# Kernel tuning notes

Hardware: AMD Instinct MI355X
Metric: run time of the kernel (lower is better)

The kernel has to match this reference:

```python
import jax, jax.numpy as jnp
import numpy as np

N_NODES = 100000
N_EDGES = 600000
N_GRAPHS = 64
BN_EPS = 1e-5


def setup_inputs() -> dict:
    key = jax.random.key(0)
    ks = jax.random.split(key, 32)
    inp = {
        "x": jax.random.normal(ks[0], (N_NODES, 128), dtype=jnp.float32),
        "edge_index": jax.random.randint(ks[1], (2, N_EDGES), 0, N_NODES, dtype=jnp.int64),
        "batch": jnp.sort(jax.random.randint(ks[2], (N_NODES,), 0, N_GRAPHS, dtype=jnp.int64)),
    }
    dims = [(128, 64, 64), (64, 64, 64), (64, 64, 96)]  # (in, hid, out) per GIN layer
    ki = 3
    for i, (d_in, d_hid, d_out) in enumerate(dims):
        inp[f"l{i}_w1"] = jax.random.normal(ks[ki], (d_in, d_hid), dtype=jnp.float32) * 0.05; ki += 1
        inp[f"l{i}_b1"] = jnp.zeros((d_hid,), dtype=jnp.float32)
        inp[f"l{i}_w2"] = jax.random.normal(ks[ki], (d_hid, d_out), dtype=jnp.float32) * 0.05; ki += 1
        inp[f"l{i}_b2"] = jnp.zeros((d_out,), dtype=jnp.float32)
        inp[f"bn{i}_g"] = jax.random.uniform(ks[ki], (d_out,), minval=0.5, maxval=1.5, dtype=jnp.float32); ki += 1
        inp[f"bn{i}_b"] = jax.random.normal(ks[ki], (d_out,), dtype=jnp.float32) * 0.05; ki += 1
        inp[f"bn{i}_m"] = jax.random.normal(ks[ki], (d_out,), dtype=jnp.float32) * 0.05; ki += 1
        inp[f"bn{i}_v"] = jax.random.uniform(ks[ki], (d_out,), minval=0.5, maxval=1.5, dtype=jnp.float32); ki += 1
    return inp


def _gin_layer(x, src, dst, w1, b1, w2, b2, g, bb, m, v):
    # GINConv (eps=0): h_i = MLP(x_i + sum_{j: j->i} x_j)
    aggr = jax.ops.segment_sum(x[src], dst, num_segments=N_NODES)
    h = x + aggr
    h = jax.nn.relu(h @ w1 + b1) @ w2 + b2
    # eval-mode BatchNorm1d + ReLU
    h = (h - m) * jax.lax.rsqrt(v + BN_EPS) * g + bb
    return jax.nn.relu(h)


def reference(x, edge_index, batch,
              l0_w1, l0_b1, l0_w2, l0_b2, bn0_g, bn0_b, bn0_m, bn0_v,
              l1_w1, l1_b1, l1_w2, l1_b2, bn1_g, bn1_b, bn1_m, bn1_v,
              l2_w1, l2_b1, l2_w2, l2_b2, bn2_g, bn2_b, bn2_m, bn2_v):
    src, dst = edge_index[0], edge_index[1]
    h = _gin_layer(x, src, dst, l0_w1, l0_b1, l0_w2, l0_b2, bn0_g, bn0_b, bn0_m, bn0_v)
    h = _gin_layer(h, src, dst, l1_w1, l1_b1, l1_w2, l1_b2, bn1_g, bn1_b, bn1_m, bn1_v)
    h = _gin_layer(h, src, dst, l2_w1, l2_b1, l2_w2, l2_b2, bn2_g, bn2_b, bn2_m, bn2_v)
    # global mean pool over graphs
    sums = jax.ops.segment_sum(h, batch, num_segments=N_GRAPHS)
    counts = jax.ops.segment_sum(jnp.ones((h.shape[0],), dtype=h.dtype), batch, num_segments=N_GRAPHS)
    return sums / jnp.maximum(counts, 1.0)[:, None]
```

## Files before the change

kernel.cpp:

```cpp
#include <hip/hip_runtime.h>

#define N_NODES 100000
#define N_GRAPHS 64
#define N_EDGES 600000
#define BN_EPS 1e-5f

__global__ void deg_hist_kernel(const int* __restrict__ dst,
                                int* __restrict__ deg, int n_edges) {
    int e = blockIdx.x * blockDim.x + threadIdx.x;
    if (e < n_edges) atomicAdd(&deg[dst[e]], 1);
}

__global__ void scan1_kernel(const int* __restrict__ deg, int* __restrict__ excl,
                             int* __restrict__ partials, int n) {
    __shared__ int s[1024];
    int i = blockIdx.x * 1024 + threadIdx.x;
    int v = (i < n) ? deg[i] : 0;
    s[threadIdx.x] = v;
    __syncthreads();
    for (int off = 1; off < 1024; off <<= 1) {
        int t = (threadIdx.x >= (unsigned)off) ? s[threadIdx.x - off] : 0;
        __syncthreads();
        s[threadIdx.x] += t;
        __syncthreads();
    }
    if (i < n) excl[i] = s[threadIdx.x] - v;
    if (threadIdx.x == 1023) partials[blockIdx.x] = s[1023];
}

__global__ void scan2_kernel(int* partials, int nb) {
    __shared__ int s[128];
    int t = threadIdx.x;
    int v = (t < nb) ? partials[t] : 0;
    s[t] = v;
    __syncthreads();
    for (int off = 1; off < 128; off <<= 1) {
        int u = (t >= off) ? s[t - off] : 0;
        __syncthreads();
        s[t] += u;
        __syncthreads();
    }
    if (t < nb) partials[t] = s[t] - v;
}

__global__ void scan3_kernel(int* __restrict__ rowptr, const int* __restrict__ partials,
                             int n, int total) {
    int i = blockIdx.x * blockDim.x + threadIdx.x;
    if (i < n) rowptr[i] += partials[i >> 10];
    else if (i == n) rowptr[n] = total;
}

__global__ void csr_fill_kernel(const int* __restrict__ src, const int* __restrict__ dst,
                                const int* __restrict__ rowptr, int* __restrict__ cursor,
                                int* __restrict__ eids, int n_edges) {
    int e = blockIdx.x * blockDim.x + threadIdx.x;
    if (e >= n_edges) return;
    int t = dst[e];
    int pos = rowptr[t] + atomicAdd(&cursor[t], 1);
    eids[pos] = src[e];
}

__global__ void graph_bounds_kernel(const int* __restrict__ batch,
                                    int* __restrict__ gstart, int n_nodes) {
    int n = blockIdx.x * blockDim.x + threadIdx.x;
    if (n >= n_nodes) return;
    if (n == 0) {
        for (int g = 0; g <= batch[0]; ++g) gstart[g] = 0;
    } else {
        int b0 = batch[n - 1], b1 = batch[n];
        for (int g = b0 + 1; g <= b1; ++g) gstart[g] = n;
    }
    if (n == n_nodes - 1) {
        for (int g = batch[n] + 1; g <= N_GRAPHS; ++g) gstart[g] = n_nodes;
    }
}

__global__ void prep_kernel(const float* __restrict__ w1, const float* __restrict__ w2,
                            const float* __restrict__ b2, const float* __restrict__ g,
                            const float* __restrict__ bb, const float* __restrict__ m,
                            const float* __restrict__ v,
                            float* __restrict__ w1T, float* __restrict__ w2sT,
                            float* __restrict__ bias2, int DIN, int DOUT) {
    int i = blockIdx.x * blockDim.x + threadIdx.x;
    if (i < 64 * DIN) {
        int j = i / DIN, k = i % DIN;
        w1T[i] = w1[k * 64 + j];
    }
    int i2 = i - 64 * DIN;
    if (i2 >= 0 && i2 < DOUT * 64) {
        int c = i2 / 64, j = i2 % 64;
        float s = g[c] * rsqrtf(v[c] + BN_EPS);
        w2sT[i2] = w2[j * DOUT + c] * s;
    }
    int i3 = i2 - DOUT * 64;
    if (i3 >= 0 && i3 < DOUT) {
        float s = g[i3] * rsqrtf(v[i3] + BN_EPS);
        bias2[i3] = (b2[i3] - m[i3]) * s + bb[i3];
    }
}

__global__ __launch_bounds__(256)
void pre_gemm_kernel(const float* __restrict__ x, const float* __restrict__ w1T,
                     float* __restrict__ y, int n_nodes) {
    __shared__ float w1s[64 * 128];
    const int tid = threadIdx.x;
    const long base = (long)blockIdx.x * 64;

    const float4* gw1 = (const float4*)w1T;
    for (int i4 = tid; i4 < 16 * 128; i4 += 256) {
        int row = i4 >> 5, k4 = i4 & 31;
        *(float4*)&w1s[row * 128 + ((k4 ^ ((row >> 2) & 7)) << 2)] = gw1[i4];
    }
    __syncthreads();

    const int jg = tid & 15, ng = tid >> 4, xw = jg & 7;
    const float* wp = &w1s[(jg * 4) * 128];
    const float4* xv = (const float4*)x;
    long r[4];
    #pragma unroll
    for (int i = 0; i < 4; ++i) {
        long rr = base + ng * 4 + i;
        r[i] = (rr < n_nodes) ? rr : (n_nodes - 1);
    }
    float acc[4][4] = {};
    #pragma unroll 4
    for (int k4 = 0; k4 < 32; ++k4) {
        const int ko = (k4 ^ xw) << 2;
        float4 w0 = *(const float4*)&wp[0 * 128 + ko];
        float4 w1v = *(const float4*)&wp[1 * 128 + ko];
        float4 w2v = *(const float4*)&wp[2 * 128 + ko];
        float4 w3v = *(const float4*)&wp[3 * 128 + ko];
        #pragma unroll
        for (int i = 0; i < 4; ++i) {
            float4 a = xv[r[i] * 32 + k4];
            acc[i][0] = fmaf(a.x, w0.x, fmaf(a.y, w0.y, fmaf(a.z, w0.z, fmaf(a.w, w0.w, acc[i][0]))));
            acc[i][1] = fmaf(a.x, w1v.x, fmaf(a.y, w1v.y, fmaf(a.z, w1v.z, fmaf(a.w, w1v.w, acc[i][1]))));
            acc[i][2] = fmaf(a.x, w2v.x, fmaf(a.y, w2v.y, fmaf(a.z, w2v.z, fmaf(a.w, w2v.w, acc[i][2]))));
            acc[i][3] = fmaf(a.x, w3v.x, fmaf(a.y, w3v.y, fmaf(a.z, w3v.z, fmaf(a.w, w3v.w, acc[i][3]))));
        }
    }
    #pragma unroll
    for (int i = 0; i < 4; ++i) {
        long n = base + ng * 4 + i;
        if (n < n_nodes) {
            float4 v = {acc[i][0], acc[i][1], acc[i][2], acc[i][3]};
            *(float4*)(y + n * 64 + jg * 4) = v;
        }
    }
}

__global__ __launch_bounds__(256)
void gather64_kernel(const float* __restrict__ y, const int* __restrict__ rowptr,
                     const int* __restrict__ eids, const float* __restrict__ b1,
                     float* __restrict__ t, int n_nodes) {
    int node = blockIdx.x * 16 + (threadIdx.x >> 4);
    if (node >= n_nodes) return;
    int f4 = threadIdx.x & 15;
    const float4* yv = (const float4*)y;
    float4 acc = yv[(long)node * 16 + f4];
    int b = rowptr[node], e = rowptr[node + 1];
    int i = b;
    for (; i + 3 < e; i += 4) {
        int s0 = eids[i], s1 = eids[i + 1], s2 = eids[i + 2], s3 = eids[i + 3];
        float4 r0 = yv[(long)s0 * 16 + f4];
        float4 r1 = yv[(long)s1 * 16 + f4];
        float4 r2 = yv[(long)s2 * 16 + f4];
        float4 r3 = yv[(long)s3 * 16 + f4];
        acc.x += (r0.x + r1.x) + (r2.x + r3.x);
        acc.y += (r0.y + r1.y) + (r2.y + r3.y);
        acc.z += (r0.z + r1.z) + (r2.z + r3.z);
        acc.w += (r0.w + r1.w) + (r2.w + r3.w);
    }
    for (; i < e; ++i) {
        int s = eids[i];
        float4 r = yv[(long)s * 16 + f4];
        acc.x += r.x; acc.y += r.y; acc.z += r.z; acc.w += r.w;
    }
    float4 bv = ((const float4*)b1)[f4];
    float4 o;
    o.x = fmaxf(acc.x + bv.x, 0.0f);
    o.y = fmaxf(acc.y + bv.y, 0.0f);
    o.z = fmaxf(acc.z + bv.z, 0.0f);
    o.w = fmaxf(acc.w + bv.w, 0.0f);
    ((float4*)t)[(long)node * 16 + f4] = o;
}

__global__ __launch_bounds__(256)
void fused_mid_kernel(const float* __restrict__ t, const float* __restrict__ w2sT,
                      const float* __restrict__ bias2, const float* __restrict__ w1nT,
                      float* __restrict__ ynext, int n_nodes) {
    constexpr int SS = 68;
    __shared__ float sT[64 * SS];
    __shared__ float wbuf[64 * 64];
    const int tid = threadIdx.x;
    const long base = (long)blockIdx.x * 64;

    const float4* gw2 = (const float4*)w2sT;
    for (int i4 = tid; i4 < 16 * 64; i4 += 256) {
        int row = i4 >> 4, k4 = i4 & 15;
        *(float4*)&wbuf[row * 64 + ((k4 ^ ((row >> 2) & 7)) << 2)] = gw2[i4];
    }
    __syncthreads();

    const int jg = tid & 15, ng = tid >> 4, xw = jg & 7;
    const float4* tv = (const float4*)(t + base * 64);

    float h[4][4];
    {
        const float* wp = &wbuf[(jg * 4) * 64];
        float acc[4][4] = {};
        #pragma unroll 4
        for (int k4 = 0; k4 < 16; ++k4) {
            const int ko = (k4 ^ xw) << 2;
            float4 w0 = *(const float4*)&wp[0 * 64 + ko];
            float4 w1v = *(const float4*)&wp[1 * 64 + ko];
            float4 w2v = *(const float4*)&wp[2 * 64 + ko];
            float4 w3v = *(const float4*)&wp[3 * 64 + ko];
            #pragma unroll
            for (int i = 0; i < 4; ++i) {
                float4 a = tv[(ng * 4 + i) * 16 + k4];
                acc[i][0] = fmaf(a.x, w0.x, fmaf(a.y, w0.y, fmaf(a.z, w0.z, fmaf(a.w, w0.w, acc[i][0]))));
                acc[i][1] = fmaf(a.x, w1v.x, fmaf(a.y, w1v.y, fmaf(a.z, w1v.z, fmaf(a.w, w1v.w, acc[i][1]))));
                acc[i][2] = fmaf(a.x, w2v.x, fmaf(a.y, w2v.y, fmaf(a.z, w2v.z, fmaf(a.w, w2v.w, acc[i][2]))));
                acc[i][3] = fmaf(a.x, w3v.x, fmaf(a.y, w3v.y, fmaf(a.z, w3v.z, fmaf(a.w, w3v.w, acc[i][3]))));
            }
        }
        float4 bv = *(const float4*)&bias2[jg * 4];
        #pragma unroll
        for (int i = 0; i < 4; ++i) {
            h[i][0] = fmaxf(acc[i][0] + bv.x, 0.0f);
            h[i][1] = fmaxf(acc[i][1] + bv.y, 0.0f);
            h[i][2] = fmaxf(acc[i][2] + bv.z, 0.0f);
            h[i][3] = fmaxf(acc[i][3] + bv.w, 0.0f);
        }
    }
    __syncthreads();

    #pragma unroll
    for (int i = 0; i < 4; ++i) {
        float4 hv = {h[i][0], h[i][1], h[i][2], h[i][3]};
        *(float4*)&sT[(ng * 4 + i) * SS + jg * 4] = hv;
    }
    const float4* gw1n = (const float4*)w1nT;
    for (int i4 = tid; i4 < 16 * 64; i4 += 256) {
        int row = i4 >> 4, k4 = i4 & 15;
        *(float4*)&wbuf[row * 64 + ((k4 ^ ((row >> 2) & 7)) << 2)] = gw1n[i4];
    }
    __syncthreads();

    {
        const float* ap = &sT[(ng * 4) * SS];
        const float* wp = &wbuf[(jg * 4) * 64];
        float acc[4][4] = {};
        #pragma unroll 4
        for (int k4 = 0; k4 < 16; ++k4) {
            const int ko = (k4 ^ xw) << 2;
            float4 w0 = *(const float4*)&wp[0 * 64 + ko];
            float4 w1v = *(const float4*)&wp[1 * 64 + ko];
            float4 w2v = *(const float4*)&wp[2 * 64 + ko];
            float4 w3v = *(const float4*)&wp[3 * 64 + ko];
            #pragma unroll
            for (int i = 0; i < 4; ++i) {
                float4 a = *(const float4*)&ap[i * SS + k4 * 4];
                acc[i][0] = fmaf(a.x, w0.x, fmaf(a.y, w0.y, fmaf(a.z, w0.z, fmaf(a.w, w0.w, acc[i][0]))));
                acc[i][1] = fmaf(a.x, w1v.x, fmaf(a.y, w1v.y, fmaf(a.z, w1v.z, fmaf(a.w, w1v.w, acc[i][1]))));
                acc[i][2] = fmaf(a.x, w2v.x, fmaf(a.y, w2v.y, fmaf(a.z, w2v.z, fmaf(a.w, w2v.w, acc[i][2]))));
                acc[i][3] = fmaf(a.x, w3v.x, fmaf(a.y, w3v.y, fmaf(a.z, w3v.z, fmaf(a.w, w3v.w, acc[i][3]))));
            }
        }
        #pragma unroll
        for (int i = 0; i < 4; ++i) {
            long n = base + ng * 4 + i;
            if (n < n_nodes) {
                float4 v = {acc[i][0], acc[i][1], acc[i][2], acc[i][3]};
                *(float4*)(ynext + n * 64 + jg * 4) = v;
            }
        }
    }
}

__global__ __launch_bounds__(256)
void fused_final_kernel(const float* __restrict__ t, const float* __restrict__ w2sT,
                        const float* __restrict__ bias2, float* __restrict__ out,
                        int n_nodes) {
    constexpr int CPT = 6;
    __shared__ float w2s[96 * 64];
    const int tid = threadIdx.x;
    const long base = (long)blockIdx.x * 64;

    const float4* gw2 = (const float4*)w2sT;
    for (int i4 = tid; i4 < 96 * 16; i4 += 256) {
        int row = i4 >> 4, k4 = i4 & 15;
        *(float4*)&w2s[row * 64 + ((k4 ^ ((row / CPT) & 7)) << 2)] = gw2[i4];
    }
    __syncthreads();

    const int cg = tid & 15, ng = tid >> 4, xw = cg & 7;
    const float4* tv = (const float4*)(t + base * 64);
    const float* wp = &w2s[(cg * CPT) * 64];
    float acc[4][CPT] = {};
    #pragma unroll 4
    for (int k4 = 0; k4 < 16; ++k4) {
        const int ko = (k4 ^ xw) << 2;
        float4 wv[CPT];
        #pragma unroll
        for (int c = 0; c < CPT; ++c) wv[c] = *(const float4*)&wp[c * 64 + ko];
        #pragma unroll
        for (int i = 0; i < 4; ++i) {
            float4 h = tv[(ng * 4 + i) * 16 + k4];
            #pragma unroll
            for (int c = 0; c < CPT; ++c)
                acc[i][c] = fmaf(h.x, wv[c].x, fmaf(h.y, wv[c].y, fmaf(h.z, wv[c].z, fmaf(h.w, wv[c].w, acc[i][c]))));
        }
    }
    float bv[CPT];
    #pragma unroll
    for (int c = 0; c < CPT; ++c) bv[c] = bias2[cg * CPT + c];
    #pragma unroll
    for (int i = 0; i < 4; ++i) {
        long n = base + ng * 4 + i;
        if (n < n_nodes) {
            float* op = out + n * 96 + cg * CPT;
            #pragma unroll
            for (int c = 0; c < CPT; ++c) op[c] = fmaxf(acc[i][c] + bv[c], 0.0f);
        }
    }
}

#define POOL_SPLIT 16
__global__ __launch_bounds__(192)
void pool_seg_kernel(const float* __restrict__ h, const int* __restrict__ gstart,
                     float* __restrict__ sums) {
    int g = blockIdx.x >> 4;
    int s = blockIdx.x & 15;
    int lo = gstart[g], hi = gstart[g + 1];
    int len = hi - lo;
    int seg = (len + POOL_SPLIT - 1) / POOL_SPLIT;
    int a = lo + s * seg;
    int b = a + seg; if (b > hi) b = hi;

    int f4 = threadIdx.x % 24;
    int chain = threadIdx.x / 24;
    const float4* hv = (const float4*)h;
    float4 acc = {0.0f, 0.0f, 0.0f, 0.0f};
    for (int n = a + chain; n < b; n += 8) {
        float4 v = hv[(long)n * 24 + f4];
        acc.x += v.x; acc.y += v.y; acc.z += v.z; acc.w += v.w;
    }
    __shared__ float4 red[8][24];
    red[chain][f4] = acc;
    __syncthreads();
    if (threadIdx.x < 24) {
        float4 t = red[0][threadIdx.x];
        #pragma unroll
        for (int c = 1; c < 8; ++c) {
            float4 r = red[c][threadIdx.x];
            t.x += r.x; t.y += r.y; t.z += r.z; t.w += r.w;
        }
        float* sp = &sums[g * 96 + threadIdx.x * 4];
        atomicAdd(sp + 0, t.x);
        atomicAdd(sp + 1, t.y);
        atomicAdd(sp + 2, t.z);
        atomicAdd(sp + 3, t.w);
    }
}

__global__ void finalize_kernel(const float* __restrict__ sums,
                                const int* __restrict__ gstart,
                                float* __restrict__ out) {
    int i = blockIdx.x * blockDim.x + threadIdx.x;
    if (i >= N_GRAPHS * 96) return;
    int g = i / 96;
    float cnt = (float)(gstart[g + 1] - gstart[g]);
    out[i] = sums[i] / fmaxf(cnt, 1.0f);
}

static inline int cdiv_l(long a, int b) { return (int)((a + b - 1) / b); }

extern "C" void kernel_launch(void* const* d_in, const int* in_sizes, int n_in,
                              void* d_out, int out_size, void* d_ws, size_t ws_size,
                              hipStream_t stream) {
    const float* x     = (const float*)d_in[0];
    const int*   ei    = (const int*)d_in[1];
    const int*   src   = ei;
    const int*   dst   = ei + N_EDGES;
    const int*   batch = (const int*)d_in[2];

    const float* P[3][8];
    int p = 3;
    for (int l = 0; l < 3; ++l)
        for (int q = 0; q < 8; ++q)
            P[l][q] = (const float*)d_in[p++];

    const long NP = N_NODES + 64;
    float* ws   = (float*)d_ws;
    float* yT   = ws;
    float* gB   = yT + NP * 64;
    float* h2   = gB + NP * 64;
    float* q    = h2 + NP * 96;
    float* w1T[3], *w2sT[3], *bias2[3];
    for (int l = 0; l < 3; ++l) {
        w1T[l] = q;   q += 64 * 128;
        w2sT[l] = q;  q += 96 * 64;
        bias2[l] = q; q += 96;
    }
    float* sums   = q;
    int* gstart   = (int*)(sums + N_GRAPHS * 96);
    int* deg      = gstart + 72;
    int* cursor   = deg + N_NODES;
    int* partials = cursor + N_NODES;
    int* rowptr   = partials + 128;
    int* eids     = rowptr + (N_NODES + 1);

    const int B = 256;
    const int DIN[3]  = {128, 64, 64};
    const int DOUT[3] = {64, 64, 96};

    for (int l = 0; l < 3; ++l) {
        int tot = 64 * DIN[l] + 64 * DOUT[l] + DOUT[l];
        prep_kernel<<<cdiv_l(tot, B), B, 0, stream>>>(
            P[l][0], P[l][2], P[l][3], P[l][4], P[l][5], P[l][6], P[l][7],
            w1T[l], w2sT[l], bias2[l], DIN[l], DOUT[l]);
    }

    hipMemsetAsync(deg, 0, (size_t)(2 * N_NODES + 128) * sizeof(int), stream);
    deg_hist_kernel<<<cdiv_l(N_EDGES, B), B, 0, stream>>>(dst, deg, N_EDGES);
    int nblk = cdiv_l(N_NODES, 1024);
    scan1_kernel<<<nblk, 1024, 0, stream>>>(deg, rowptr, partials, N_NODES);
    scan2_kernel<<<1, 128, 0, stream>>>(partials, nblk);
    scan3_kernel<<<cdiv_l(N_NODES + 1, B), B, 0, stream>>>(rowptr, partials, N_NODES, N_EDGES);
    csr_fill_kernel<<<cdiv_l(N_EDGES, B), B, 0, stream>>>(src, dst, rowptr, cursor, eids, N_EDGES);
    graph_bounds_kernel<<<cdiv_l(N_NODES, B), B, 0, stream>>>(batch, gstart, N_NODES);

    const int ntiles = cdiv_l(N_NODES, 64);
    const int ngather = cdiv_l(N_NODES, 16);

    pre_gemm_kernel<<<ntiles, 256, 0, stream>>>(x, w1T[0], yT, N_NODES);
    gather64_kernel<<<ngather, 256, 0, stream>>>(yT, rowptr, eids, P[0][1], gB, N_NODES);
    fused_mid_kernel<<<ntiles, 256, 0, stream>>>(
        gB, w2sT[0], bias2[0], w1T[1], yT, N_NODES);
    gather64_kernel<<<ngather, 256, 0, stream>>>(yT, rowptr, eids, P[1][1], gB, N_NODES);
    fused_mid_kernel<<<ntiles, 256, 0, stream>>>(
        gB, w2sT[1], bias2[1], w1T[2], yT, N_NODES);
    gather64_kernel<<<ngather, 256, 0, stream>>>(yT, rowptr, eids, P[2][1], gB, N_NODES);
    fused_final_kernel<<<ntiles, 256, 0, stream>>>(
        gB, w2sT[2], bias2[2], h2, N_NODES);

    hipMemsetAsync(sums, 0, (size_t)(N_GRAPHS * 96) * sizeof(float), stream);
    pool_seg_kernel<<<N_GRAPHS * POOL_SPLIT, 192, 0, stream>>>(h2, gstart, sums);
    finalize_kernel<<<cdiv_l(N_GRAPHS * 96, B), B, 0, stream>>>(
        sums, gstart, (float*)d_out);
}
```

Before: 433.4 us.

## Store gathered features in bf16 and merge small setup kernels

The intermediate per-node features that the gather kernels read are now written and read as bf16, which halves the bytes fetched in the random-access neighbour gathers. The three per-layer prep kernels become one 2D-grid launch, and the CSR fill and graph-bounds kernels are merged into one. Pooling writes per-block partials instead of using atomics and a memset, and finalize sums those partials. The bf16 storage adds rounding error to the aggregated activations, and y is now double-buffered.

New measurement: 395.1 us. 1.1x faster.

```diff
diff --git a/kernel.cpp b/kernel.cpp
--- a/kernel.cpp
+++ b/kernel.cpp
@@ -4,6 +4,28 @@
 #define N_GRAPHS 64
 #define N_EDGES 600000
 #define BN_EPS 1e-5f
+
+typedef unsigned short bf16_t;
+
+__device__ __forceinline__ unsigned short f2bf(float f) {
+    unsigned int u = __float_as_uint(f);
+    u += 0x7FFF + ((u >> 16) & 1);
+    return (unsigned short)(u >> 16);
+}
+__device__ __forceinline__ float4 bf2f4(uint2 p) {
+    float4 r;
+    r.x = __uint_as_float(p.x << 16);
+    r.y = __uint_as_float(p.x & 0xFFFF0000u);
+    r.z = __uint_as_float(p.y << 16);
+    r.w = __uint_as_float(p.y & 0xFFFF0000u);
+    return r;
+}
+__device__ __forceinline__ uint2 pack4(float a, float b, float c, float d) {
+    uint2 p;
+    p.x = (unsigned)f2bf(a) | ((unsigned)f2bf(b) << 16);
+    p.y = (unsigned)f2bf(c) | ((unsigned)f2bf(d) << 16);
+    return p;
+}
 
 __global__ void deg_hist_kernel(const int* __restrict__ dst,
                                 int* __restrict__ deg, int n_edges) {
@@ -50,58 +72,59 @@
     else if (i == n) rowptr[n] = total;
 }
 
-__global__ void csr_fill_kernel(const int* __restrict__ src, const int* __restrict__ dst,
-                                const int* __restrict__ rowptr, int* __restrict__ cursor,
-                                int* __restrict__ eids, int n_edges) {
+__global__ void fill_bounds_kernel(const int* __restrict__ src, const int* __restrict__ dst,
+                                   const int* __restrict__ rowptr, int* __restrict__ cursor,
+                                   int* __restrict__ eids, const int* __restrict__ batch,
+                                   int* __restrict__ gstart, int n_edges, int n_nodes) {
     int e = blockIdx.x * blockDim.x + threadIdx.x;
-    if (e >= n_edges) return;
-    int t = dst[e];
-    int pos = rowptr[t] + atomicAdd(&cursor[t], 1);
-    eids[pos] = src[e];
-}
-
-__global__ void graph_bounds_kernel(const int* __restrict__ batch,
-                                    int* __restrict__ gstart, int n_nodes) {
-    int n = blockIdx.x * blockDim.x + threadIdx.x;
-    if (n >= n_nodes) return;
-    if (n == 0) {
-        for (int g = 0; g <= batch[0]; ++g) gstart[g] = 0;
-    } else {
-        int b0 = batch[n - 1], b1 = batch[n];
-        for (int g = b0 + 1; g <= b1; ++g) gstart[g] = n;
-    }
-    if (n == n_nodes - 1) {
-        for (int g = batch[n] + 1; g <= N_GRAPHS; ++g) gstart[g] = n_nodes;
-    }
-}
-
-__global__ void prep_kernel(const float* __restrict__ w1, const float* __restrict__ w2,
-                            const float* __restrict__ b2, const float* __restrict__ g,
-                            const float* __restrict__ bb, const float* __restrict__ m,
-                            const float* __restrict__ v,
-                            float* __restrict__ w1T, float* __restrict__ w2sT,
-                            float* __restrict__ bias2, int DIN, int DOUT) {
+    if (e < n_edges) {
+        int t = dst[e];
+        int pos = rowptr[t] + atomicAdd(&cursor[t], 1);
+        eids[pos] = src[e];
+    }
+    if (e < n_nodes) {
+        if (e == 0) {
+            for (int g = 0; g <= batch[0]; ++g) gstart[g] = 0;
+        } else {
+            int b0 = batch[e - 1], b1 = batch[e];
+            for (int g = b0 + 1; g <= b1; ++g) gstart[g] = e;
+        }
+        if (e == n_nodes - 1) {
+            for (int g = batch[e] + 1; g <= N_GRAPHS; ++g) gstart[g] = n_nodes;
+        }
+    }
+}
+
+struct LayerPrep {
+    const float *w1, *w2, *b2, *g, *bb, *m, *v;
+    float *w1T, *w2sT, *bias2;
+    int DIN, DOUT;
+};
+struct PrepAll { LayerPrep l[3]; };
+
+__global__ void prep_all_kernel(PrepAll pa) {
+    LayerPrep P = pa.l[blockIdx.y];
     int i = blockIdx.x * blockDim.x + threadIdx.x;
-    if (i < 64 * DIN) {
-        int j = i / DIN, k = i % DIN;
-        w1T[i] = w1[k * 64 + j];
-    }
-    int i2 = i - 64 * DIN;
-    if (i2 >= 0 && i2 < DOUT * 64) {
+    if (i < 64 * P.DIN) {
+        int j = i / P.DIN, k = i % P.DIN;
+        P.w1T[i] = P.w1[k * 64 + j];
+    }
+    int i2 = i - 64 * P.DIN;
+    if (i2 >= 0 && i2 < P.DOUT * 64) {
         int c = i2 / 64, j = i2 % 64;
-        float s = g[c] * rsqrtf(v[c] + BN_EPS);
-        w2sT[i2] = w2[j * DOUT + c] * s;
-    }
-    int i3 = i2 - DOUT * 64;
-    if (i3 >= 0 && i3 < DOUT) {
-        float s = g[i3] * rsqrtf(v[i3] + BN_EPS);
-        bias2[i3] = (b2[i3] - m[i3]) * s + bb[i3];
+        float s = P.g[c] * rsqrtf(P.v[c] + BN_EPS);
+        P.w2sT[i2] = P.w2[j * P.DOUT + c] * s;
+    }
+    int i3 = i2 - P.DOUT * 64;
+    if (i3 >= 0 && i3 < P.DOUT) {
+        float s = P.g[i3] * rsqrtf(P.v[i3] + BN_EPS);
+        P.bias2[i3] = (P.b2[i3] - P.m[i3]) * s + P.bb[i3];
     }
 }
 
 __global__ __launch_bounds__(256)
 void pre_gemm_kernel(const float* __restrict__ x, const float* __restrict__ w1T,
-                     float* __restrict__ y, int n_nodes) {
+                     bf16_t* __restrict__ y, int n_nodes) {
     __shared__ float w1s[64 * 128];
     const int tid = threadIdx.x;
     const long base = (long)blockIdx.x * 64;
@@ -143,29 +166,29 @@
     for (int i = 0; i < 4; ++i) {
         long n = base + ng * 4 + i;
         if (n < n_nodes) {
-            float4 v = {acc[i][0], acc[i][1], acc[i][2], acc[i][3]};
-            *(float4*)(y + n * 64 + jg * 4) = v;
+            *(uint2*)(y + n * 64 + jg * 4) = pack4(acc[i][0], acc[i][1], acc[i][2], acc[i][3]);
         }
     }
 }
 
 __global__ __launch_bounds__(256)
-void gather64_kernel(const float* __restrict__ y, const int* __restrict__ rowptr,
+void gather64_kernel(const bf16_t* __restrict__ y, const int* __restrict__ rowptr,
                      const int* __restrict__ eids, const float* __restrict__ b1,
                      float* __restrict__ t, int n_nodes) {
     int node = blockIdx.x * 16 + (threadIdx.x >> 4);
     if (node >= n_nodes) return;
     int f4 = threadIdx.x & 15;
-    const float4* yv = (const float4*)y;
-    float4 acc = yv[(long)node * 16 + f4];
+    const uint2* yv = (const uint2*)y;
+    float4 acc = bf2f4(yv[(long)node * 16 + f4]);
     int b = rowptr[node], e = rowptr[node + 1];
     int i = b;
     for (; i + 3 < e; i += 4) {
         int s0 = eids[i], s1 = eids[i + 1], s2 = eids[i + 2], s3 = eids[i + 3];
-        float4 r0 = yv[(long)s0 * 16 + f4];
-        float4 r1 = yv[(long)s1 * 16 + f4];
-        float4 r2 = yv[(long)s2 * 16 + f4];
-        float4 r3 = yv[(long)s3 * 16 + f4];
+        uint2 q0 = yv[(long)s0 * 16 + f4];
+        uint2 q1 = yv[(long)s1 * 16 + f4];
+        uint2 q2 = yv[(long)s2 * 16 + f4];
+        uint2 q3 = yv[(long)s3 * 16 + f4];
+        float4 r0 = bf2f4(q0), r1 = bf2f4(q1), r2 = bf2f4(q2), r3 = bf2f4(q3);
         acc.x += (r0.x + r1.x) + (r2.x + r3.x);
         acc.y += (r0.y + r1.y) + (r2.y + r3.y);
         acc.z += (r0.z + r1.z) + (r2.z + r3.z);
@@ -173,7 +196,7 @@
     }
     for (; i < e; ++i) {
         int s = eids[i];
-        float4 r = yv[(long)s * 16 + f4];
+        float4 r = bf2f4(yv[(long)s * 16 + f4]);
         acc.x += r.x; acc.y += r.y; acc.z += r.z; acc.w += r.w;
     }
     float4 bv = ((const float4*)b1)[f4];
@@ -188,7 +211,7 @@
 __global__ __launch_bounds__(256)
 void fused_mid_kernel(const float* __restrict__ t, const float* __restrict__ w2sT,
                       const float* __restrict__ bias2, const float* __restrict__ w1nT,
-                      float* __restrict__ ynext, int n_nodes) {
+                      bf16_t* __restrict__ ynext, int n_nodes) {
     constexpr int SS = 68;
     __shared__ float sT[64 * SS];
     __shared__ float wbuf[64 * 64];
@@ -272,8 +295,7 @@
         for (int i = 0; i < 4; ++i) {
             long n = base + ng * 4 + i;
             if (n < n_nodes) {
-                float4 v = {acc[i][0], acc[i][1], acc[i][2], acc[i][3]};
-                *(float4*)(ynext + n * 64 + jg * 4) = v;
+                *(uint2*)(ynext + n * 64 + jg * 4) = pack4(acc[i][0], acc[i][1], acc[i][2], acc[i][3]);
             }
         }
     }
@@ -330,7 +352,7 @@
 #define POOL_SPLIT 16
 __global__ __launch_bounds__(192)
 void pool_seg_kernel(const float* __restrict__ h, const int* __restrict__ gstart,
-                     float* __restrict__ sums) {
+                     float* __restrict__ part) {
     int g = blockIdx.x >> 4;
     int s = blockIdx.x & 15;
     int lo = gstart[g], hi = gstart[g + 1];
@@ -357,22 +379,21 @@
             float4 r = red[c][threadIdx.x];
             t.x += r.x; t.y += r.y; t.z += r.z; t.w += r.w;
         }
-        float* sp = &sums[g * 96 + threadIdx.x * 4];
-        atomicAdd(sp + 0, t.x);
-        atomicAdd(sp + 1, t.y);
-        atomicAdd(sp + 2, t.z);
-        atomicAdd(sp + 3, t.w);
-    }
-}
-
-__global__ void finalize_kernel(const float* __restrict__ sums,
+        *(float4*)&part[((long)blockIdx.x) * 96 + threadIdx.x * 4] = t;
+    }
+}
+
+__global__ void finalize_kernel(const float* __restrict__ part,
                                 const int* __restrict__ gstart,
                                 float* __restrict__ out) {
     int i = blockIdx.x * blockDim.x + threadIdx.x;
     if (i >= N_GRAPHS * 96) return;
-    int g = i / 96;
+    int g = i / 96, c = i - g * 96;
+    float s = 0.0f;
+    #pragma unroll
+    for (int k = 0; k < POOL_SPLIT; ++k) s += part[((long)g * POOL_SPLIT + k) * 96 + c];
     float cnt = (float)(gstart[g + 1] - gstart[g]);
-    out[i] = sums[i] / fmaxf(cnt, 1.0f);
+    out[i] = s / fmaxf(cnt, 1.0f);
 }
 
 static inline int cdiv_l(long a, int b) { return (int)((a + b - 1) / b); }
@@ -393,9 +414,10 @@
             P[l][q] = (const float*)d_in[p++];
 
     const long NP = N_NODES + 64;
-    float* ws   = (float*)d_ws;
-    float* yT   = ws;
-    float* gB   = yT + NP * 64;
+    char* wsb   = (char*)d_ws;
+    bf16_t* yA  = (bf16_t*)wsb;
+    bf16_t* yB  = yA + NP * 64;
+    float* gB   = (float*)(yB + NP * 64);
     float* h2   = gB + NP * 64;
     float* q    = h2 + NP * 96;
     float* w1T[3], *w2sT[3], *bias2[3];
@@ -404,8 +426,8 @@
         w2sT[l] = q;  q += 96 * 64;
         bias2[l] = q; q += 96;
     }
-    float* sums   = q;
-    int* gstart   = (int*)(sums + N_GRAPHS * 96);
+    float* part   = q;
+    int* gstart   = (int*)(part + N_GRAPHS * POOL_SPLIT * 96);
     int* deg      = gstart + 72;
     int* cursor   = deg + N_NODES;
     int* partials = cursor + N_NODES;
@@ -416,12 +438,16 @@
     const int DIN[3]  = {128, 64, 64};
     const int DOUT[3] = {64, 64, 96};
 
+    PrepAll pa;
     for (int l = 0; l < 3; ++l) {
-        int tot = 64 * DIN[l] + 64 * DOUT[l] + DOUT[l];
-        prep_kernel<<<cdiv_l(tot, B), B, 0, stream>>>(
-            P[l][0], P[l][2], P[l][3], P[l][4], P[l][5], P[l][6], P[l][7],
-            w1T[l], w2sT[l], bias2[l], DIN[l], DOUT[l]);
-    }
+        pa.l[l].w1 = P[l][0]; pa.l[l].w2 = P[l][2]; pa.l[l].b2 = P[l][3];
+        pa.l[l].g = P[l][4];  pa.l[l].bb = P[l][5]; pa.l[l].m = P[l][6];
+        pa.l[l].v = P[l][7];
+        pa.l[l].w1T = w1T[l]; pa.l[l].w2sT = w2sT[l]; pa.l[l].bias2 = bias2[l];
+        pa.l[l].DIN = DIN[l]; pa.l[l].DOUT = DOUT[l];
+    }
+    dim3 pgrid(cdiv_l(64 * 128 + 96 * 64 + 96, B), 3);
+    prep_all_kernel<<<pgrid, B, 0, stream>>>(pa);
 
     hipMemsetAsync(deg, 0, (size_t)(2 * N_NODES + 128) * sizeof(int), stream);
     deg_hist_kernel<<<cdiv_l(N_EDGES, B), B, 0, stream>>>(dst, deg, N_EDGES);
@@ -429,25 +455,24 @@
     scan1_kernel<<<nblk, 1024, 0, stream>>>(deg, rowptr, partials, N_NODES);
     scan2_kernel<<<1, 128, 0, stream>>>(partials, nblk);
     scan3_kernel<<<cdiv_l(N_NODES + 1, B), B, 0, stream>>>(rowptr, partials, N_NODES, N_EDGES);
-    csr_fill_kernel<<<cdiv_l(N_EDGES, B), B, 0, stream>>>(src, dst, rowptr, cursor, eids, N_EDGES);
-    graph_bounds_kernel<<<cdiv_l(N_NODES, B), B, 0, stream>>>(batch, gstart, N_NODES);
+    fill_bounds_kernel<<<cdiv_l(N_EDGES, B), B, 0, stream>>>(
+        src, dst, rowptr, cursor, eids, batch, gstart, N_EDGES, N_NODES);
 
     const int ntiles = cdiv_l(N_NODES, 64);
     const int ngather = cdiv_l(N_NODES, 16);
 
-    pre_gemm_kernel<<<ntiles, 256, 0, stream>>>(x, w1T[0], yT, N_NODES);
-    gather64_kernel<<<ngather, 256, 0, stream>>>(yT, rowptr, eids, P[0][1], gB, N_NODES);
+    pre_gemm_kernel<<<ntiles, 256, 0, stream>>>(x, w1T[0], yA, N_NODES);
+    gather64_kernel<<<ngather, 256, 0, stream>>>(yA, rowptr, eids, P[0][1], gB, N_NODES);
     fused_mid_kernel<<<ntiles, 256, 0, stream>>>(
-        gB, w2sT[0], bias2[0], w1T[1], yT, N_NODES);
-    gather64_kernel<<<ngather, 256, 0, stream>>>(yT, rowptr, eids, P[1][1], gB, N_NODES);
+        gB, w2sT[0], bias2[0], w1T[1], yB, N_NODES);
+    gather64_kernel<<<ngather, 256, 0, stream>>>(yB, rowptr, eids, P[1][1], gB, N_NODES);
     fused_mid_kernel<<<ntiles, 256, 0, stream>>>(
-        gB, w2sT[1], bias2[1], w1T[2], yT, N_NODES);
-    gather64_kernel<<<ngather, 256, 0, stream>>>(yT, rowptr, eids, P[2][1], gB, N_NODES);
+        gB, w2sT[1], bias2[1], w1T[2], yA, N_NODES);
+    gather64_kernel<<<ngather, 256, 0, stream>>>(yA, rowptr, eids, P[2][1], gB, N_NODES);
     fused_final_kernel<<<ntiles, 256, 0, stream>>>(
         gB, w2sT[2], bias2[2], h2, N_NODES);
 
-    hipMemsetAsync(sums, 0, (size_t)(N_GRAPHS * 96) * sizeof(float), stream);
-    pool_seg_kernel<<<N_GRAPHS * POOL_SPLIT, 192, 0, stream>>>(h2, gstart, sums);
+    pool_seg_kernel<<<N_GRAPHS * POOL_SPLIT, 192, 0, stream>>>(h2, gstart, part);
     finalize_kernel<<<cdiv_l(N_GRAPHS * 96, B), B, 0, stream>>>(
-        sums, gstart, (float*)d_out);
-}
+        part, gstart, (float*)d_out);
+}
```
